# Kernel tuning notes

Hardware: AMD Instinct MI355X
Metric: run time of the kernel (lower is better)

The kernel has to match this reference:

```python
import jax, jax.numpy as jnp
import numpy as np

B, T, IN, H, L, CS, OUT = 256, 256, 256, 1024, 8, 10, 64
CHUNK = H // L


def setup_inputs() -> dict:
    key = jax.random.key(0)
    ks = jax.random.split(key, 16)
    G = 4 * H + 2 * L
    s = 0.05
    return {
        "x": jax.random.normal(ks[0], (B, T, IN), jnp.float32),
        "time": jax.random.uniform(ks[1], (B, T, 1), jnp.float32),
        "kernel_w": jax.random.normal(ks[2], (IN + 1, G), jnp.float32) * s,
        "kernel_b": jnp.zeros((G,), jnp.float32),
        "rec_w": jax.random.normal(ks[3], (H + 1, G), jnp.float32) * s,
        "rec_b": jnp.zeros((G,), jnp.float32),
        "scale_w": jax.random.normal(ks[4], (H, H // 6), jnp.float32) * s,
        "scale_b": jnp.zeros((H // 6,), jnp.float32),
        "rescale_w": jax.random.normal(ks[5], (H // 6, H), jnp.float32) * s,
        "rescale_b": jnp.zeros((H,), jnp.float32),
        "conv_w": jax.random.normal(ks[6], (H, H, CS), jnp.float32) * s,  # (out_ch, in_ch, k)
        "conv_b": jnp.zeros((H,), jnp.float32),
        "out_w": jax.random.normal(ks[7], (H, OUT), jnp.float32) * s,
        "out_b": jnp.zeros((OUT,), jnp.float32),
    }


def _stagenet(x, time, kernel_w, kernel_b, rec_w, rec_b, scale_w, scale_b,
              rescale_w, rescale_b, conv_w, conv_b, out_w, out_b):
    batch = x.shape[0]

    def step(carry, xt):
        c, h, tmp_h, tmp_dis = carry
        inp, intv = xt  # (B,IN), (B,1)
        xo = (jnp.concatenate([inp, intv], -1) @ kernel_w + kernel_b
              + jnp.concatenate([h, intv], -1) @ rec_w + rec_b)  # (B, 4H+2L)
        # master gates via cumax
        fm = jnp.cumsum(jax.nn.softmax(xo[:, :L], axis=-1), axis=-1)            # l2r (B,L)
        im_sm = jax.nn.softmax(xo[:, L:2 * L], axis=-1)
        im = jnp.flip(jnp.cumsum(jnp.flip(im_sm, -1), axis=-1), -1)             # r2l (B,L)
        g = xo[:, 2 * L:].reshape(batch, 4 * L, CHUNK)
        f_g = jax.nn.sigmoid(g[:, :L])
        i_g = jax.nn.sigmoid(g[:, L:2 * L])
        o_g = jax.nn.sigmoid(g[:, 2 * L:3 * L])
        c_in = jnp.tanh(g[:, 3 * L:])
        c_l = c.reshape(batch, L, CHUNK)
        fmE, imE = fm[:, :, None], im[:, :, None]
        ov = fmE * imE
        c_new = ov * (f_g * c_l + i_g * c_in) + (fmE - ov) * c_l + (imE - ov) * c_in
        h_new = (o_g * jnp.tanh(c_new)).reshape(batch, H)
        c_new = c_new.reshape(batch, H)
        cur_dis = 1.0 - jnp.mean(fm, -1)                                        # (B,)
        # sliding window buffers
        tmp_h = jnp.concatenate([tmp_h[1:], h_new[None]], 0)                    # (CS,B,H)
        tmp_dis = jnp.concatenate([tmp_dis[1:], cur_dis[None]], 0)              # (CS,B)
        # cumsum-softmax local attention over the window
        ld = jax.nn.softmax(jnp.cumsum(tmp_dis.T, axis=1), axis=1)              # (B,CS)
        lh = tmp_h.transpose(1, 2, 0) * ld[:, None, :]                          # (B,H,CS)
        theme = jnp.mean(lh, -1) @ scale_w + scale_b
        theme = jax.nn.sigmoid(jax.nn.relu(theme) @ rescale_w + rescale_b)      # (B,H)
        conv_out = jnp.einsum('bck,ock->bo', lh, conv_w) + conv_b               # conv1d, out len 1
        local_h = theme * conv_out
        return (c_new, h_new, tmp_h, tmp_dis), (h_new, local_h, cur_dis)

    c0 = jnp.zeros((batch, H), x.dtype)
    h0 = jnp.zeros((batch, H), x.dtype)
    tmp_h0 = jnp.zeros((CS, batch, H), x.dtype)
    tmp_dis0 = jnp.zeros((CS, batch), x.dtype)
    xs = (x.transpose(1, 0, 2), time.transpose(1, 0, 2))
    _, (origin_h, local_h, distance) = jax.lax.scan(step, (c0, h0, tmp_h0, tmp_dis0), xs)
    rnn = (local_h + origin_h).transpose(1, 0, 2)                               # (B,T,H)
    output = jax.nn.sigmoid(rnn @ out_w + out_b)                                # (B,T,OUT)
    return output, distance  # distance: (T,B)


def reference(x, time, kernel_w, kernel_b, rec_w, rec_b, scale_w, scale_b,
              rescale_w, rescale_b, conv_w, conv_b, out_w, out_b):
    return _stagenet(x, time, kernel_w, kernel_b, rec_w, rec_b, scale_w, scale_b,
                     rescale_w, rescale_b, conv_w, conv_b, out_w, out_b)
```

## Files before the change

kernel.cpp:

```cpp
#include <hip/hip_runtime.h>
#include <hip/hip_bf16.h>
#include <math.h>

#define BB 256
#define TT 256
#define INW 256
#define HH 1024
#define LL 8
#define CSW 10
#define OUTW 64
#define GG 4112
#define KSEG 1344
#define NPAD 4224
#define BH (BB * HH)
#define NPANEL 66

typedef __attribute__((ext_vector_type(8))) short short8;
typedef __attribute__((ext_vector_type(4))) float f32x4;

__device__ __forceinline__ float bf2f(ushort u) {
    union { float f; unsigned int i; } v; v.i = ((unsigned int)u) << 16; return v.f;
}
__device__ __forceinline__ ushort f2bf(float f) {
    __hip_bfloat16 h = __float2bfloat16(f);
    return *(ushort*)&h;
}
__device__ __forceinline__ float sigf(float v) { return 1.0f / (1.0f + expf(-v)); }

template<int WR, int WC, int AMODE, int EPI>
__global__ __launch_bounds__(WR * WC * 64) void mm_kernel(
    const ushort* __restrict__ A, const float* __restrict__ xf,
    const float* __restrict__ tf, const ushort* __restrict__ hR,
    const ushort* __restrict__ hLo,
    const ushort* __restrict__ BT, const float* __restrict__ bias,
    void* __restrict__ Cp, const float* __restrict__ ldw,
    const ushort* __restrict__ TH, float* __restrict__ outp,
    int splitStride, int ldaA, int ldb, int ldc, int K, int t, int RING, int tBase)
{
    constexpr int BM = WR * 64, BN = WC * 64, NT = WR * WC * 64, LS = 72;
    constexpr int AIT = BM * 8 / NT, BIT = BN * 8 / NT;
    __shared__ ushort As[BM * LS];
    __shared__ ushort Bs[BN * LS];
    const int tid = threadIdx.x;
    const int lane = tid & 63, wave = tid >> 6;
    const int wr = wave / WC, wc = wave % WC;

    int bx, by, zSel = 0;
    const ushort* BTeff = BT;
    if (AMODE == 1) {
        int vid = blockIdx.x;
        int xcd = vid & 7, q = vid >> 3;
        int p = -1, mem = 0;
        for (int j = 0; ; ++j) {
            int pp = xcd + 8 * j;
            if (pp >= NPANEL) break;
            int cc = (pp < 33) ? 4 : 2;
            if (q < cc) { p = pp; mem = q; break; }
            q -= cc;
        }
        if (p < 0) return;
        if (p < 33) { bx = p;      zSel = (mem < 2) ? 0 : 2; by = mem & 1; BTeff = BT; }
        else        { bx = p - 33; zSel = 1;                 by = mem & 1; BTeff = A;  }
    } else {
        bx = blockIdx.x; by = blockIdx.y;
    }
    const int m0 = by * BM, n0 = bx * BN;
    f32x4 acc[4][4] = {};

    auto gather = [&](int ktl, short8* vA, short8* vB) {
#pragma unroll
        for (int i = 0; i < AIT; ++i) {
            int id = tid + i * NT;
            int r = id >> 3, cc = id & 7;
            int k = ktl + cc * 8;
            short8 v;
            if (AMODE == 0) {
                v = *(const short8*)(A + (size_t)(m0 + r) * ldaA + k);
            } else if (AMODE == 1) {
                bool lo = (zSel == 2);
                if (k < 288) {
                    float xv[8];
                    int b = m0 + r;
                    if (k < 256) {
                        const float* src = xf + ((size_t)b * TT + t) * INW + k;
#pragma unroll
                        for (int j = 0; j < 8; ++j) xv[j] = src[j];
                    } else if (k == 256) {
                        float tv = tf[(size_t)b * TT + t];
                        xv[0] = tv; xv[1] = tv;
#pragma unroll
                        for (int j = 2; j < 8; ++j) xv[j] = 0.f;
                    } else {
#pragma unroll
                        for (int j = 0; j < 8; ++j) xv[j] = 0.f;
                    }
                    ushort* po = (ushort*)&v;
#pragma unroll
                    for (int j = 0; j < 8; ++j) {
                        ushort hi = f2bf(xv[j]);
                        po[j] = lo ? f2bf(xv[j] - bf2f(hi)) : hi;
                    }
                } else if (k < 1312) {
                    const ushort* src = lo
                        ? hLo + (size_t)(m0 + r) * HH + (k - 288)
                        : hR + (size_t)((t + 8) % RING) * BH + (size_t)(m0 + r) * HH + (k - 288);
                    v = *(const short8*)src;
                } else {
                    ushort* pz = (ushort*)&v;
#pragma unroll
                    for (int j = 0; j < 8; ++j) pz[j] = 0;
                }
            } else {
                int ks = k >> 10, c = k & 1023;
                int tt = m0 >> 8, b = (m0 & 255) + r;
                int slot = (tBase + tt + ks) % RING;
                short8 hv = *(const short8*)(hR + (size_t)slot * BH + (size_t)b * HH + c);
                float s = ldw[((size_t)tt * 256 + b) * CSW + ks];
                ushort* pv = (ushort*)&hv;
                ushort* po = (ushort*)&v;
#pragma unroll
                for (int j = 0; j < 8; ++j) po[j] = f2bf(bf2f(pv[j]) * s);
            }
            vA[i] = v;
        }
#pragma unroll
        for (int i = 0; i < BIT; ++i) {
            int id = tid + i * NT;
            int n = id >> 3, cc = id & 7;
            vB[i] = *(const short8*)(BTeff + (size_t)(n0 + n) * ldb + ktl + cc * 8);
        }
    };

    short8 vA[AIT], vB[BIT];
    gather(0, vA, vB);

    for (int kt = 0; kt < K; kt += 64) {
#pragma unroll
        for (int i = 0; i < AIT; ++i) {
            int id = tid + i * NT;
            *(short8*)(As + (id >> 3) * LS + (id & 7) * 8) = vA[i];
        }
#pragma unroll
        for (int i = 0; i < BIT; ++i) {
            int id = tid + i * NT;
            *(short8*)(Bs + (id >> 3) * LS + (id & 7) * 8) = vB[i];
        }
        __syncthreads();
        if (kt + 64 < K) gather(kt + 64, vA, vB);
#pragma unroll
        for (int kf = 0; kf < 2; ++kf) {
            short8 aF[4], bF[4];
#pragma unroll
            for (int mi = 0; mi < 4; ++mi)
                aF[mi] = *(const short8*)(As + (wr * 64 + mi * 16 + (lane & 15)) * LS + kf * 32 + (lane >> 4) * 8);
#pragma unroll
            for (int ni = 0; ni < 4; ++ni)
                bF[ni] = *(const short8*)(Bs + (wc * 64 + ni * 16 + (lane & 15)) * LS + kf * 32 + (lane >> 4) * 8);
#pragma unroll
            for (int mi = 0; mi < 4; ++mi)
#pragma unroll
                for (int ni = 0; ni < 4; ++ni)
                    acc[mi][ni] = __builtin_amdgcn_mfma_f32_16x16x32_bf16(aF[mi], bF[ni], acc[mi][ni], 0, 0, 0);
        }
        __syncthreads();
    }
#pragma unroll
    for (int mi = 0; mi < 4; ++mi) {
#pragma unroll
        for (int ni = 0; ni < 4; ++ni) {
#pragma unroll
            for (int j = 0; j < 4; ++j) {
                int row = m0 + wr * 64 + mi * 16 + ((lane >> 4) << 2) + j;
                int col = n0 + wc * 64 + ni * 16 + (lane & 15);
                float v = acc[mi][ni][j];
                if (EPI != 0 && bias) v += bias[col];
                if (EPI == 0) {
                    ((float*)Cp)[(size_t)zSel * splitStride + (size_t)row * ldc + col] = v;
                } else if (EPI == 1) {
                    ((ushort*)Cp)[(size_t)row * ldc + col] = f2bf(v > 0.f ? v : 0.f);
                } else if (EPI == 2) {
                    ((ushort*)Cp)[(size_t)row * ldc + col] = f2bf(sigf(v));
                } else if (EPI == 3) {
                    int tt = row >> 8, b = row & 255;
                    int slot = (tBase + tt + 9) % RING;
                    float th = bf2f(TH[(size_t)row * HH + col]);
                    float h  = bf2f(hR[(size_t)slot * BH + (size_t)b * HH + col]);
                    ((ushort*)Cp)[(size_t)row * ldc + col] = f2bf(th * v + h);
                } else {
                    int tt = tBase + (row >> 8), b = row & 255;
                    outp[((size_t)b * TT + tt) * OUTW + col] = sigf(v);
                }
            }
        }
    }
}

__global__ void build_whl(const float* __restrict__ kw, const float* __restrict__ rw,
                          ushort* __restrict__ WhiT, ushort* __restrict__ WloT)
{
    size_t i = (size_t)blockIdx.x * 256 + threadIdx.x;
    if (i >= (size_t)NPAD * KSEG) return;
    int n = (int)(i / KSEG), k = (int)(i % KSEG);
    float w = 0.f;
    if (n < GG) {
        if (k < 256)           w = kw[(size_t)k * GG + n];
        else if (k == 256)     w = kw[(size_t)256 * GG + n];
        else if (k == 257)     w = rw[(size_t)1024 * GG + n];
        else if (k >= 288 && k < 1312) w = rw[(size_t)(k - 288) * GG + n];
    }
    ushort hi = f2bf(w);
    WhiT[i] = hi;
    WloT[i] = f2bf(w - bf2f(hi));
}

__global__ void build_bc(const float* __restrict__ kb, const float* __restrict__ rb,
                         float* __restrict__ bc)
{
    int i = blockIdx.x * 256 + threadIdx.x;
    if (i < NPAD) bc[i] = (i < GG) ? kb[i] + rb[i] : 0.f;
}

__global__ void build_ctt(const float* __restrict__ cw, ushort* __restrict__ ctT)
{
    size_t i = (size_t)blockIdx.x * 256 + threadIdx.x;
    if (i >= (size_t)HH * HH * CSW) return;
    int o = (int)(i / (HH * CSW)), rest = (int)(i % (HH * CSW));
    int k = rest >> 10, c = rest & 1023;
    ctT[i] = f2bf(cw[((size_t)o * HH + c) * CSW + k]);
}

__global__ void build_swt(const float* __restrict__ sw, const float* __restrict__ sb,
                          ushort* __restrict__ swT, float* __restrict__ sbP)
{
    int i = blockIdx.x * 256 + threadIdx.x;
    if (i < 256 * 1024) {
        int n = i >> 10, k = i & 1023;
        swT[i] = f2bf(n < 170 ? sw[(size_t)k * 170 + n] : 0.f);
    }
    if (i < 256) sbP[i] = (i < 170) ? sb[i] : 0.f;
}

__global__ void build_rswt(const float* __restrict__ rsw, ushort* __restrict__ rswT)
{
    int i = blockIdx.x * 256 + threadIdx.x;
    if (i >= 1024 * 256) return;
    int n = i >> 8, k = i & 255;
    rswT[i] = f2bf(k < 170 ? rsw[(size_t)k * HH + n] : 0.f);
}

__global__ void build_owt(const float* __restrict__ ow, ushort* __restrict__ owT)
{
    int i = blockIdx.x * 256 + threadIdx.x;
    if (i >= OUTW * HH) return;
    int n = i >> 10, k = i & 1023;
    owT[i] = f2bf(ow[(size_t)k * OUTW + n]);
}

__global__ __launch_bounds__(256) void step_kernel(
    const float* __restrict__ xoP, const float* __restrict__ bc,
    float* __restrict__ c, ushort* __restrict__ hR, ushort* __restrict__ hLo,
    float* __restrict__ dist, int t, int RING)
{
    const size_t S = (size_t)BB * NPAD;
    int b = blockIdx.x, tid = threadIdx.x;
    const float* x0 = xoP + (size_t)b * NPAD;
    __shared__ float fm[LL], im[LL];
    if (tid == 0) {
        float xr[2 * LL];
        for (int l = 0; l < 2 * LL; ++l) xr[l] = x0[l] + x0[S + l] + x0[2 * S + l] + bc[l];
        float m1 = -1e30f, m2 = -1e30f;
        for (int l = 0; l < LL; ++l) { m1 = fmaxf(m1, xr[l]); m2 = fmaxf(m2, xr[LL + l]); }
        float e1[LL], e2[LL], s1 = 0.f, s2 = 0.f;
        for (int l = 0; l < LL; ++l) {
            e1[l] = expf(xr[l] - m1); s1 += e1[l];
            e2[l] = expf(xr[LL + l] - m2); s2 += e2[l];
        }
        float cum = 0.f, mean = 0.f;
        for (int l = 0; l < LL; ++l) { cum += e1[l] / s1; fm[l] = cum; mean += cum; }
        float rc = 0.f;
        for (int l = LL - 1; l >= 0; --l) { rc += e2[l] / s2; im[l] = rc; }
        dist[(size_t)t * BB + b] = 1.0f - mean / LL;
    }
    __syncthreads();
    int slot = (t + 9) % RING;
    for (int e = tid; e < HH; e += 256) {
        int l = e >> 7;
        int c0 = 2 * LL + e;
        float f  = sigf(x0[c0] + x0[S + c0] + x0[2 * S + c0] + bc[c0]);
        int c1 = c0 + HH;
        float ig = sigf(x0[c1] + x0[S + c1] + x0[2 * S + c1] + bc[c1]);
        int c2 = c1 + HH;
        float og = sigf(x0[c2] + x0[S + c2] + x0[2 * S + c2] + bc[c2]);
        int c3 = c2 + HH;
        float ci = tanhf(x0[c3] + x0[S + c3] + x0[2 * S + c3] + bc[c3]);
        size_t idx = (size_t)b * HH + e;
        float cl = c[idx];
        float F = fm[l], I = im[l], OV = F * I;
        float cn = OV * (f * cl + ig * ci) + (F - OV) * cl + (I - OV) * ci;
        float hn = og * tanhf(cn);
        c[idx] = cn;
        ushort hi = f2bf(hn);
        hR[(size_t)slot * BH + idx] = hi;
        hLo[idx] = f2bf(hn - bf2f(hi));
    }
}

__global__ void ld_chunk_kernel(const float* __restrict__ dist, float* __restrict__ ldC,
                                int tBase, int Mloc)
{
    int id = blockIdx.x * 256 + threadIdx.x;
    if (id >= Mloc) return;
    int t = tBase + (id >> 8), b = id & 255;
    float cv[CSW], cum = 0.f, mx = -1e30f;
#pragma unroll
    for (int k = 0; k < CSW; ++k) {
        int ts = t - 9 + k;
        cum += (ts >= 0) ? dist[(size_t)ts * BB + b] : 0.f;
        cv[k] = cum; mx = fmaxf(mx, cum);
    }
    float ss = 0.f;
#pragma unroll
    for (int k = 0; k < CSW; ++k) { cv[k] = expf(cv[k] - mx); ss += cv[k]; }
    float inv = 1.0f / ss;
#pragma unroll
    for (int k = 0; k < CSW; ++k) ldC[(size_t)id * CSW + k] = cv[k] * inv;
}

__global__ void mlh_kernel(const ushort* __restrict__ hR, const float* __restrict__ ldC,
                           ushort* __restrict__ MLH, int tBase, int RING)
{
    size_t id = (size_t)blockIdx.x * 256 + threadIdx.x;
    int m = (int)(id >> 7);
    int c0 = ((int)(id & 127)) << 3;
    int t = tBase + (m >> 8), b = m & 255;
    float acc[8] = {};
#pragma unroll
    for (int k = 0; k < CSW; ++k) {
        float s = ldC[(size_t)m * CSW + k];
        int slot = (t + k) % RING;
        short8 hv = *(const short8*)(hR + (size_t)slot * BH + (size_t)b * HH + c0);
        ushort* pv = (ushort*)&hv;
#pragma unroll
        for (int j = 0; j < 8; ++j) acc[j] += bf2f(pv[j]) * s;
    }
#pragma unroll
    for (int j = 0; j < 8; ++j) MLH[(size_t)m * HH + c0 + j] = f2bf(acc[j] * 0.1f);
}

extern "C" void kernel_launch(void* const* d_in, const int* in_sizes, int n_in,
                              void* d_out, int out_size, void* d_ws, size_t ws_size,
                              hipStream_t stream)
{
    const float* x   = (const float*)d_in[0];
    const float* tim = (const float*)d_in[1];
    const float* kw  = (const float*)d_in[2];
    const float* kb  = (const float*)d_in[3];
    const float* rw  = (const float*)d_in[4];
    const float* rb  = (const float*)d_in[5];
    const float* sw  = (const float*)d_in[6];
    const float* sb  = (const float*)d_in[7];
    const float* rsw = (const float*)d_in[8];
    const float* rsb = (const float*)d_in[9];
    const float* cw  = (const float*)d_in[10];
    const float* cb  = (const float*)d_in[11];
    const float* ow  = (const float*)d_in[12];
    const float* ob  = (const float*)d_in[13];
    float* out  = (float*)d_out;
    float* dist = out + (size_t)BB * TT * OUTW;

    auto planSize = [&](int tch) -> size_t {
        size_t o = 0;
        auto al = [&](size_t bytes) { o += (bytes + 255) & ~(size_t)255; };
        int ring = tch + 9;
        al((size_t)ring * BH * 2);
        al((size_t)BH * 2);
        al((size_t)BH * 4);
        al((size_t)NPAD * KSEG * 2);
        al((size_t)NPAD * KSEG * 2);
        al((size_t)NPAD * 4);
        al((size_t)3 * BB * NPAD * 4);
        al((size_t)tch * 256 * CSW * 4);
        al((size_t)HH * HH * CSW * 2);
        al((size_t)256 * 1024 * 2);
        al((size_t)256 * 4);
        al((size_t)1024 * 256 * 2);
        al((size_t)OUTW * HH * 2);
        al((size_t)tch * 256 * HH * 2);
        al((size_t)tch * 256 * 256 * 2);
        al((size_t)tch * 256 * HH * 2);
        return o;
    };
    const int cands[5] = {64, 32, 16, 8, 4};
    int TCH = 0;
    for (int ci = 0; ci < 5; ++ci)
        if (planSize(cands[ci]) <= ws_size) { TCH = cands[ci]; break; }
    if (TCH == 0) return;
    const int RING = TCH + 9;
    const int Mloc = TCH * 256;

    char* base = (char*)d_ws;
    size_t off = 0;
    auto alloc = [&](size_t bytes) { char* p = base + off; off += (bytes + 255) & ~(size_t)255; return p; };
    ushort* hRing = (ushort*)alloc((size_t)RING * BH * 2);
    ushort* hLo   = (ushort*)alloc((size_t)BH * 2);
    float*  c     = (float*) alloc((size_t)BH * 4);
    ushort* WhiT  = (ushort*)alloc((size_t)NPAD * KSEG * 2);
    ushort* WloT  = (ushort*)alloc((size_t)NPAD * KSEG * 2);
    float*  bc    = (float*) alloc((size_t)NPAD * 4);
    float*  xoP   = (float*) alloc((size_t)3 * BB * NPAD * 4);
    float*  ldC   = (float*) alloc((size_t)TCH * 256 * CSW * 4);
    ushort* ctT   = (ushort*)alloc((size_t)HH * HH * CSW * 2);
    ushort* swT   = (ushort*)alloc((size_t)256 * 1024 * 2);
    float*  sbP   = (float*) alloc((size_t)256 * 4);
    ushort* rswT  = (ushort*)alloc((size_t)1024 * 256 * 2);
    ushort* owT   = (ushort*)alloc((size_t)OUTW * HH * 2);
    ushort* MLH   = (ushort*)alloc((size_t)TCH * 256 * HH * 2);
    ushort* TH1   = (ushort*)alloc((size_t)TCH * 256 * 256 * 2);
    ushort* TH    = (ushort*)alloc((size_t)TCH * 256 * HH * 2);
    ushort* RNN   = MLH;

    hipMemsetAsync(hRing, 0, (size_t)9 * BH * 2, stream);
    hipMemsetAsync(hLo, 0, (size_t)BH * 2, stream);
    hipMemsetAsync(c, 0, (size_t)BH * 4, stream);

    build_whl<<<(int)(((size_t)NPAD * KSEG + 255) / 256), 256, 0, stream>>>(kw, rw, WhiT, WloT);
    build_bc<<<(NPAD + 255) / 256, 256, 0, stream>>>(kb, rb, bc);
    build_ctt<<<(int)(((size_t)HH * HH * CSW + 255) / 256), 256, 0, stream>>>(cw, ctT);
    build_swt<<<(256 * 1024 + 255) / 256, 256, 0, stream>>>(sw, sb, swT, sbP);
    build_rswt<<<(1024 * 256 + 255) / 256, 256, 0, stream>>>(rsw, rswT);
    build_owt<<<(OUTW * HH + 255) / 256, 256, 0, stream>>>(ow, owT);

    const int SPLIT_STRIDE = BB * NPAD;

    for (int tBase = 0; tBase < TT; tBase += TCH) {
        for (int t = tBase; t < tBase + TCH; ++t) {
            mm_kernel<2, 2, 1, 0><<<dim3(224), 256, 0, stream>>>(
                WloT, x, tim, hRing, hLo, WhiT, nullptr, xoP, nullptr, nullptr, nullptr,
                SPLIT_STRIDE, 0, KSEG, NPAD, KSEG, t, RING, 0);
            step_kernel<<<BB, 256, 0, stream>>>(xoP, bc, c, hRing, hLo, dist, t, RING);
        }
        ld_chunk_kernel<<<Mloc / 256, 256, 0, stream>>>(dist, ldC, tBase, Mloc);
        mlh_kernel<<<Mloc / 2, 256, 0, stream>>>(hRing, ldC, MLH, tBase, RING);
        mm_kernel<2, 2, 0, 1><<<dim3(2, Mloc / 128), 256, 0, stream>>>(
            MLH, nullptr, nullptr, nullptr, nullptr, swT, sbP, TH1, nullptr, nullptr, nullptr,
            0, 1024, 1024, 256, 1024, 0, RING, tBase);
        mm_kernel<2, 2, 0, 2><<<dim3(8, Mloc / 128), 256, 0, stream>>>(
            TH1, nullptr, nullptr, nullptr, nullptr, rswT, rsb, TH, nullptr, nullptr, nullptr,
            0, 256, 256, 1024, 256, 0, RING, tBase);
        mm_kernel<2, 2, 2, 3><<<dim3(8, Mloc / 128), 256, 0, stream>>>(
            nullptr, nullptr, nullptr, hRing, nullptr, ctT, cb, RNN, ldC, TH, nullptr,
            0, 0, HH * CSW, 1024, HH * CSW, 0, RING, tBase);
        mm_kernel<4, 1, 0, 4><<<dim3(1, Mloc / 256), 256, 0, stream>>>(
            RNN, nullptr, nullptr, nullptr, nullptr, owT, ob, nullptr, nullptr, nullptr, out,
            0, 1024, 1024, 0, 1024, 0, RING, tBase);
    }
}
```

Before: 12.38 ms.

## Hoist input projection out of recurrence into batched chunk GEMM

Moves the x/time part of the gate pre-activation (kernel_w term) out of the per-timestep split-bf16 GEMM. It is now computed once per time chunk as one large GEMM, with the hi/lo split packed along K, into a new xoX buffer that step_kernel adds in. The per-step GEMM shrinks from K=1344 to K=1024 and its A loads become plain vector loads. The cost is extra workspace, which lowers the chunk size candidates from 64 to 32. The conv GEMM launch also gets an XCD-aware tile remap.

```diff
diff --git a/kernel.cpp b/kernel.cpp
--- a/kernel.cpp
+++ b/kernel.cpp
@@ -10,7 +10,8 @@
 #define CSW 10
 #define OUTW 64
 #define GG 4112
-#define KSEG 1344
+#define KH 1024
+#define KXP 896
 #define NPAD 4224
 #define BH (BB * HH)
 #define NPANEL 66
@@ -29,8 +30,7 @@
 
 template<int WR, int WC, int AMODE, int EPI>
 __global__ __launch_bounds__(WR * WC * 64) void mm_kernel(
-    const ushort* __restrict__ A, const float* __restrict__ xf,
-    const float* __restrict__ tf, const ushort* __restrict__ hR,
+    const ushort* __restrict__ A, const ushort* __restrict__ hR,
     const ushort* __restrict__ hLo,
     const ushort* __restrict__ BT, const float* __restrict__ bias,
     void* __restrict__ Cp, const float* __restrict__ ldw,
@@ -47,6 +47,7 @@
 
     int bx, by, zSel = 0;
     const ushort* BTeff = BT;
+    const ushort* Abase = A;
     if (AMODE == 1) {
         int vid = blockIdx.x;
         int xcd = vid & 7, q = vid >> 3;
@@ -61,6 +62,12 @@
         if (p < 0) return;
         if (p < 33) { bx = p;      zSel = (mem < 2) ? 0 : 2; by = mem & 1; BTeff = BT; }
         else        { bx = p - 33; zSel = 1;                 by = mem & 1; BTeff = A;  }
+        Abase = (zSel == 2) ? hLo : hR + (size_t)((t + 8) % RING) * BH;
+    } else if (AMODE == 2) {
+        int vid = blockIdx.x;
+        bx = (vid >> 3) & 7;
+        by = ((vid >> 6) << 3) + (vid & 7);
+        if (by >= t) return;
     } else {
         bx = blockIdx.x; by = blockIdx.y;
     }
@@ -77,39 +84,7 @@
             if (AMODE == 0) {
                 v = *(const short8*)(A + (size_t)(m0 + r) * ldaA + k);
             } else if (AMODE == 1) {
-                bool lo = (zSel == 2);
-                if (k < 288) {
-                    float xv[8];
-                    int b = m0 + r;
-                    if (k < 256) {
-                        const float* src = xf + ((size_t)b * TT + t) * INW + k;
-#pragma unroll
-                        for (int j = 0; j < 8; ++j) xv[j] = src[j];
-                    } else if (k == 256) {
-                        float tv = tf[(size_t)b * TT + t];
-                        xv[0] = tv; xv[1] = tv;
-#pragma unroll
-                        for (int j = 2; j < 8; ++j) xv[j] = 0.f;
-                    } else {
-#pragma unroll
-                        for (int j = 0; j < 8; ++j) xv[j] = 0.f;
-                    }
-                    ushort* po = (ushort*)&v;
-#pragma unroll
-                    for (int j = 0; j < 8; ++j) {
-                        ushort hi = f2bf(xv[j]);
-                        po[j] = lo ? f2bf(xv[j] - bf2f(hi)) : hi;
-                    }
-                } else if (k < 1312) {
-                    const ushort* src = lo
-                        ? hLo + (size_t)(m0 + r) * HH + (k - 288)
-                        : hR + (size_t)((t + 8) % RING) * BH + (size_t)(m0 + r) * HH + (k - 288);
-                    v = *(const short8*)src;
-                } else {
-                    ushort* pz = (ushort*)&v;
-#pragma unroll
-                    for (int j = 0; j < 8; ++j) pz[j] = 0;
-                }
+                v = *(const short8*)(Abase + (size_t)(m0 + r) * HH + k);
             } else {
                 int ks = k >> 10, c = k & 1023;
                 int tt = m0 >> 8, b = (m0 & 255) + r;
@@ -195,29 +170,57 @@
     }
 }
 
-__global__ void build_whl(const float* __restrict__ kw, const float* __restrict__ rw,
+__global__ void build_whl(const float* __restrict__ rw,
                           ushort* __restrict__ WhiT, ushort* __restrict__ WloT)
 {
     size_t i = (size_t)blockIdx.x * 256 + threadIdx.x;
-    if (i >= (size_t)NPAD * KSEG) return;
-    int n = (int)(i / KSEG), k = (int)(i % KSEG);
-    float w = 0.f;
-    if (n < GG) {
-        if (k < 256)           w = kw[(size_t)k * GG + n];
-        else if (k == 256)     w = kw[(size_t)256 * GG + n];
-        else if (k == 257)     w = rw[(size_t)1024 * GG + n];
-        else if (k >= 288 && k < 1312) w = rw[(size_t)(k - 288) * GG + n];
-    }
+    if (i >= (size_t)NPAD * KH) return;
+    int n = (int)(i / KH), k = (int)(i % KH);
+    float w = (n < GG) ? rw[(size_t)k * GG + n] : 0.f;
     ushort hi = f2bf(w);
     WhiT[i] = hi;
     WloT[i] = f2bf(w - bf2f(hi));
 }
 
+__global__ void build_wxt(const float* __restrict__ kw, const float* __restrict__ rw,
+                          ushort* __restrict__ WxT)
+{
+    size_t i = (size_t)blockIdx.x * 256 + threadIdx.x;
+    if (i >= (size_t)NPAD * KXP) return;
+    int n = (int)(i / KXP), k = (int)(i % KXP);
+    int seg = k / 288, kk = k - seg * 288;
+    float w = 0.f;
+    if (n < GG && seg < 3) {
+        if (kk < 256)      w = kw[(size_t)kk * GG + n];
+        else if (kk == 256) w = kw[(size_t)256 * GG + n];
+        else if (kk == 257) w = rw[(size_t)1024 * GG + n];
+    }
+    ushort hi = f2bf(w);
+    WxT[i] = (seg == 1) ? f2bf(w - bf2f(hi)) : hi;
+}
+
 __global__ void build_bc(const float* __restrict__ kb, const float* __restrict__ rb,
                          float* __restrict__ bc)
 {
     int i = blockIdx.x * 256 + threadIdx.x;
     if (i < NPAD) bc[i] = (i < GG) ? kb[i] + rb[i] : 0.f;
+}
+
+__global__ void build_xac(const float* __restrict__ x, const float* __restrict__ tim,
+                          ushort* __restrict__ XAc, int tBase, int Mloc)
+{
+    size_t i = (size_t)blockIdx.x * 256 + threadIdx.x;
+    if (i >= (size_t)Mloc * KXP) return;
+    int m = (int)(i / KXP), k = (int)(i % KXP);
+    int t = tBase + (m >> 8), b = m & 255;
+    int seg = k / 288, kk = k - seg * 288;
+    float v = 0.f;
+    if (seg < 3) {
+        if (kk < 256)       v = x[((size_t)b * TT + t) * INW + kk];
+        else if (kk < 258)  v = tim[(size_t)b * TT + t];
+    }
+    ushort hi = f2bf(v);
+    XAc[i] = (seg == 2) ? f2bf(v - bf2f(hi)) : hi;
 }
 
 __global__ void build_ctt(const float* __restrict__ cw, ushort* __restrict__ ctT)
@@ -257,17 +260,20 @@
 }
 
 __global__ __launch_bounds__(256) void step_kernel(
-    const float* __restrict__ xoP, const float* __restrict__ bc,
+    const float* __restrict__ xoP, const float* __restrict__ xoX,
+    const float* __restrict__ bc,
     float* __restrict__ c, ushort* __restrict__ hR, ushort* __restrict__ hLo,
-    float* __restrict__ dist, int t, int RING)
+    float* __restrict__ dist, int t, int tBase, int RING)
 {
     const size_t S = (size_t)BB * NPAD;
     int b = blockIdx.x, tid = threadIdx.x;
     const float* x0 = xoP + (size_t)b * NPAD;
+    const float* xx = xoX + ((size_t)(t - tBase) * 256 + b) * NPAD;
     __shared__ float fm[LL], im[LL];
     if (tid == 0) {
         float xr[2 * LL];
-        for (int l = 0; l < 2 * LL; ++l) xr[l] = x0[l] + x0[S + l] + x0[2 * S + l] + bc[l];
+        for (int l = 0; l < 2 * LL; ++l)
+            xr[l] = x0[l] + x0[S + l] + x0[2 * S + l] + xx[l] + bc[l];
         float m1 = -1e30f, m2 = -1e30f;
         for (int l = 0; l < LL; ++l) { m1 = fmaxf(m1, xr[l]); m2 = fmaxf(m2, xr[LL + l]); }
         float e1[LL], e2[LL], s1 = 0.f, s2 = 0.f;
@@ -286,13 +292,13 @@
     for (int e = tid; e < HH; e += 256) {
         int l = e >> 7;
         int c0 = 2 * LL + e;
-        float f  = sigf(x0[c0] + x0[S + c0] + x0[2 * S + c0] + bc[c0]);
+        float f  = sigf(x0[c0] + x0[S + c0] + x0[2 * S + c0] + xx[c0] + bc[c0]);
         int c1 = c0 + HH;
-        float ig = sigf(x0[c1] + x0[S + c1] + x0[2 * S + c1] + bc[c1]);
+        float ig = sigf(x0[c1] + x0[S + c1] + x0[2 * S + c1] + xx[c1] + bc[c1]);
         int c2 = c1 + HH;
-        float og = sigf(x0[c2] + x0[S + c2] + x0[2 * S + c2] + bc[c2]);
+        float og = sigf(x0[c2] + x0[S + c2] + x0[2 * S + c2] + xx[c2] + bc[c2]);
         int c3 = c2 + HH;
-        float ci = tanhf(x0[c3] + x0[S + c3] + x0[2 * S + c3] + bc[c3]);
+        float ci = tanhf(x0[c3] + x0[S + c3] + x0[2 * S + c3] + xx[c3] + bc[c3]);
         size_t idx = (size_t)b * HH + e;
         float cl = c[idx];
         float F = fm[l], I = im[l], OV = F * I;
@@ -375,10 +381,13 @@
         al((size_t)ring * BH * 2);
         al((size_t)BH * 2);
         al((size_t)BH * 4);
-        al((size_t)NPAD * KSEG * 2);
-        al((size_t)NPAD * KSEG * 2);
+        al((size_t)NPAD * KH * 2);
+        al((size_t)NPAD * KH * 2);
+        al((size_t)NPAD * KXP * 2);
         al((size_t)NPAD * 4);
         al((size_t)3 * BB * NPAD * 4);
+        al((size_t)tch * 256 * NPAD * 4);
+        al((size_t)tch * 256 * KXP * 2);
         al((size_t)tch * 256 * CSW * 4);
         al((size_t)HH * HH * CSW * 2);
         al((size_t)256 * 1024 * 2);
@@ -390,13 +399,14 @@
         al((size_t)tch * 256 * HH * 2);
         return o;
     };
-    const int cands[5] = {64, 32, 16, 8, 4};
+    const int cands[5] = {32, 16, 8, 4, 2};
     int TCH = 0;
     for (int ci = 0; ci < 5; ++ci)
         if (planSize(cands[ci]) <= ws_size) { TCH = cands[ci]; break; }
     if (TCH == 0) return;
     const int RING = TCH + 9;
     const int Mloc = TCH * 256;
+    const int nM = Mloc / 128;
 
     char* base = (char*)d_ws;
     size_t off = 0;
@@ -404,26 +414,30 @@
     ushort* hRing = (ushort*)alloc((size_t)RING * BH * 2);
     ushort* hLo   = (ushort*)alloc((size_t)BH * 2);
     float*  c     = (float*) alloc((size_t)BH * 4);
-    ushort* WhiT  = (ushort*)alloc((size_t)NPAD * KSEG * 2);
-    ushort* WloT  = (ushort*)alloc((size_t)NPAD * KSEG * 2);
+    ushort* WhiT  = (ushort*)alloc((size_t)NPAD * KH * 2);
+    ushort* WloT  = (ushort*)alloc((size_t)NPAD * KH * 2);
+    ushort* WxT   = (ushort*)alloc((size_t)NPAD * KXP * 2);
     float*  bc    = (float*) alloc((size_t)NPAD * 4);
     float*  xoP   = (float*) alloc((size_t)3 * BB * NPAD * 4);
-    float*  ldC   = (float*) alloc((size_t)TCH * 256 * CSW * 4);
+    float*  xoX   = (float*) alloc((size_t)Mloc * NPAD * 4);
+    ushort* XAc   = (ushort*)alloc((size_t)Mloc * KXP * 2);
+    float*  ldC   = (float*) alloc((size_t)Mloc * CSW * 4);
     ushort* ctT   = (ushort*)alloc((size_t)HH * HH * CSW * 2);
     ushort* swT   = (ushort*)alloc((size_t)256 * 1024 * 2);
     float*  sbP   = (float*) alloc((size_t)256 * 4);
     ushort* rswT  = (ushort*)alloc((size_t)1024 * 256 * 2);
     ushort* owT   = (ushort*)alloc((size_t)OUTW * HH * 2);
-    ushort* MLH   = (ushort*)alloc((size_t)TCH * 256 * HH * 2);
-    ushort* TH1   = (ushort*)alloc((size_t)TCH * 256 * 256 * 2);
-    ushort* TH    = (ushort*)alloc((size_t)TCH * 256 * HH * 2);
+    ushort* MLH   = (ushort*)alloc((size_t)Mloc * HH * 2);
+    ushort* TH1   = (ushort*)alloc((size_t)Mloc * 256 * 2);
+    ushort* TH    = (ushort*)alloc((size_t)Mloc * HH * 2);
     ushort* RNN   = MLH;
 
     hipMemsetAsync(hRing, 0, (size_t)9 * BH * 2, stream);
     hipMemsetAsync(hLo, 0, (size_t)BH * 2, stream);
     hipMemsetAsync(c, 0, (size_t)BH * 4, stream);
 
-    build_whl<<<(int)(((size_t)NPAD * KSEG + 255) / 256), 256, 0, stream>>>(kw, rw, WhiT, WloT);
+    build_whl<<<(int)(((size_t)NPAD * KH + 255) / 256), 256, 0, stream>>>(rw, WhiT, WloT);
+    build_wxt<<<(int)(((size_t)NPAD * KXP + 255) / 256), 256, 0, stream>>>(kw, rw, WxT);
     build_bc<<<(NPAD + 255) / 256, 256, 0, stream>>>(kb, rb, bc);
     build_ctt<<<(int)(((size_t)HH * HH * CSW + 255) / 256), 256, 0, stream>>>(cw, ctT);
     build_swt<<<(256 * 1024 + 255) / 256, 256, 0, stream>>>(sw, sb, swT, sbP);
@@ -433,25 +447,31 @@
     const int SPLIT_STRIDE = BB * NPAD;
 
     for (int tBase = 0; tBase < TT; tBase += TCH) {
+        build_xac<<<(int)(((size_t)Mloc * KXP + 255) / 256), 256, 0, stream>>>(
+            x, tim, XAc, tBase, Mloc);
+        mm_kernel<2, 2, 0, 0><<<dim3(33, Mloc / 128), 256, 0, stream>>>(
+            XAc, nullptr, nullptr, WxT, nullptr, xoX, nullptr, nullptr, nullptr,
+            0, KXP, KXP, NPAD, KXP, 0, RING, tBase);
         for (int t = tBase; t < tBase + TCH; ++t) {
             mm_kernel<2, 2, 1, 0><<<dim3(224), 256, 0, stream>>>(
-                WloT, x, tim, hRing, hLo, WhiT, nullptr, xoP, nullptr, nullptr, nullptr,
-                SPLIT_STRIDE, 0, KSEG, NPAD, KSEG, t, RING, 0);
-            step_kernel<<<BB, 256, 0, stream>>>(xoP, bc, c, hRing, hLo, dist, t, RING);
-        }
-        ld_chunk_kernel<<<Mloc / 256, 256, 0, stream>>>(dist, ldC, tBase, Mloc);
+                WloT, hRing, hLo, WhiT, nullptr, xoP, nullptr, nullptr, nullptr,
+                SPLIT_STRIDE, 0, KH, NPAD, KH, t, RING, 0);
+            step_kernel<<<BB, 256, 0, stream>>>(
+                xoP, xoX, bc, c, hRing, hLo, dist, t, tBase, RING);
+        }
+        ld_chunk_kernel<<<(Mloc + 255) / 256, 256, 0, stream>>>(dist, ldC, tBase, Mloc);
         mlh_kernel<<<Mloc / 2, 256, 0, stream>>>(hRing, ldC, MLH, tBase, RING);
         mm_kernel<2, 2, 0, 1><<<dim3(2, Mloc / 128), 256, 0, stream>>>(
-            MLH, nullptr, nullptr, nullptr, nullptr, swT, sbP, TH1, nullptr, nullptr, nullptr,
+            MLH, nullptr, nullptr, swT, sbP, TH1, nullptr, nullptr, nullptr,
             0, 1024, 1024, 256, 1024, 0, RING, tBase);
         mm_kernel<2, 2, 0, 2><<<dim3(8, Mloc / 128), 256, 0, stream>>>(
-            TH1, nullptr, nullptr, nullptr, nullptr, rswT, rsb, TH, nullptr, nullptr, nullptr,
+            TH1, nullptr, nullptr, rswT, rsb, TH, nullptr, nullptr, nullptr,
             0, 256, 256, 1024, 256, 0, RING, tBase);
-        mm_kernel<2, 2, 2, 3><<<dim3(8, Mloc / 128), 256, 0, stream>>>(
-            nullptr, nullptr, nullptr, hRing, nullptr, ctT, cb, RNN, ldC, TH, nullptr,
-            0, 0, HH * CSW, 1024, HH * CSW, 0, RING, tBase);
+        mm_kernel<2, 2, 2, 3><<<dim3(((nM + 7) / 8) * 64), 256, 0, stream>>>(
+            nullptr, hRing, nullptr, ctT, cb, RNN, ldC, TH, nullptr,
+            0, 0, HH * CSW, 1024, HH * CSW, nM, RING, tBase);
         mm_kernel<4, 1, 0, 4><<<dim3(1, Mloc / 256), 256, 0, stream>>>(
-            RNN, nullptr, nullptr, nullptr, nullptr, owT, ob, nullptr, nullptr, nullptr, out,
+            RNN, nullptr, nullptr, owT, ob, nullptr, nullptr, nullptr, out,
             0, 1024, 1024, 0, 1024, 0, RING, tBase);
     }
 }
```

New measurement: 13.05 ms. 1.05x slower.
